# Performance work log

Measured on AMD Instinct MI355X. Metric: run time of the kernel, lower is better.

Reference implementation:

```python
import jax, jax.numpy as jnp
import numpy as np

B, T, D_MODEL = 2, 2048, 1024
H, D_HEAD, R = 16, 64, 16
CAUSAL = True


def setup_inputs() -> dict:
    key = jax.random.key(0)
    ks = jax.random.split(key, 6)
    return {
        "x": jax.random.normal(ks[0], (B, T, D_MODEL), dtype=jnp.float32),
        "W_qkv": jax.random.normal(ks[1], (D_MODEL, 3 * D_MODEL), dtype=jnp.float32) * 0.02,
        "W_q_lsr": jax.random.normal(ks[2], (H, D_HEAD, R), dtype=jnp.float32) * 0.1,
        "W_k_lsr": jax.random.normal(ks[3], (H, D_HEAD, R), dtype=jnp.float32) * 0.1,
        "core": jax.random.normal(ks[4], (H, R), dtype=jnp.float32),
        "W_o": jax.random.normal(ks[5], (D_MODEL, D_MODEL), dtype=jnp.float32) * 0.02,
    }


def reference(x, W_qkv, W_q_lsr, W_k_lsr, core, W_o):
    Bx, Tx, D = x.shape
    Hh, Dh, Rr = W_q_lsr.shape
    # Fused QKV projection, then split heads -> (B, H, T, D_head)
    qkv = x @ W_qkv  # (B, T, 3D)
    q, k, v = jnp.split(qkv, 3, axis=-1)
    q = q.reshape(Bx, Tx, Hh, Dh).transpose(0, 2, 1, 3)
    k = k.reshape(Bx, Tx, Hh, Dh).transpose(0, 2, 1, 3)
    v = v.reshape(Bx, Tx, Hh, Dh).transpose(0, 2, 1, 3)
    # Low-rank (LSR) projections of q and k; core + 1/sqrt(R) scaling on q side
    scale = 1.0 / jnp.sqrt(jnp.asarray(max(Rr, 1), dtype=jnp.float32))
    q_lr = jnp.einsum('bhtd,hdr->bhtr', q, W_q_lsr) * core[None, :, None, :] * scale
    k_lr = jnp.einsum('bhtd,hdr->bhtr', k, W_k_lsr)
    # Low-rank scores (B, H, T, T)
    scores = jnp.einsum('bhir,bhjr->bhij', q_lr, k_lr)
    if CAUSAL:
        mask = jnp.tril(jnp.ones((Tx, Tx), dtype=bool))
        scores = jnp.where(mask[None, None], scores, -jnp.inf)
    attn = jax.nn.softmax(scores, axis=-1)
    out = jnp.einsum('bhij,bhjd->bhid', attn, v)  # (B, H, T, D_head)
    out = out.transpose(0, 2, 1, 3).reshape(Bx, Tx, D)
    return out @ W_o
```

## Files before the change

### kernel.cpp

```cpp
#include <hip/hip_runtime.h>
#include <hip/hip_bf16.h>

#define BB 2
#define TT 2048
#define DD 1024
#define HH 16
#define DH 64
#define RR 16
#define BT (BB*TT)
#define BH (BB*HH)
#define D3 (3*DD)
#define NC 1536

typedef __bf16 bf16x8 __attribute__((ext_vector_type(8)));
typedef float f32x4 __attribute__((ext_vector_type(4)));
typedef short short4v __attribute__((ext_vector_type(4)));

__device__ __forceinline__ float bf2f(unsigned short u) {
  unsigned int v = ((unsigned int)u) << 16;
  return __builtin_bit_cast(float, v);
}
__device__ __forceinline__ unsigned short f2bf(float f) {
  unsigned int x = __builtin_bit_cast(unsigned int, f);
  unsigned int r = x + 0x7fffu + ((x >> 16) & 1u);
  return (unsigned short)(r >> 16);
}
__device__ __forceinline__ short4v pack_bf16x4(float a, float b, float c, float d) {
  uint2 u;
  u.x = (unsigned)f2bf(a) | ((unsigned)f2bf(b) << 16);
  u.y = (unsigned)f2bf(c) | ((unsigned)f2bf(d) << 16);
  return __builtin_bit_cast(short4v, u);
}

#define NEG_BIG (-1e30f)

__device__ __forceinline__ void async_copy16(const void* g, void* l) {
  __builtin_amdgcn_global_load_lds((const __attribute__((address_space(1))) void*)g,
                                   (__attribute__((address_space(3))) void*)l, 16, 0, 0);
}

__global__ __launch_bounds__(256) void cvt_f32_bf16(const float* __restrict__ in,
                                                    unsigned short* __restrict__ out,
                                                    int n) {
  int i = (blockIdx.x * 256 + threadIdx.x) * 8;
  if (i >= n) return;
  float4 a = *(const float4*)&in[i];
  float4 b = *(const float4*)&in[i + 4];
  unsigned short t[8] = {f2bf(a.x), f2bf(a.y), f2bf(a.z), f2bf(a.w),
                         f2bf(b.x), f2bf(b.y), f2bf(b.z), f2bf(b.w)};
  *(uint4*)&out[i] = *(const uint4*)t;
}

__global__ __launch_bounds__(256) void transpose_cvt(const float* __restrict__ in,
                                                     unsigned short* __restrict__ out,
                                                     int R, int C, int coff) {
  __shared__ float tile[32][33];
  const int tx = threadIdx.x, ty = threadIdx.y;
  const int x = blockIdx.x * 32 + tx;
  const int y0 = blockIdx.y * 32;
#pragma unroll
  for (int i = 0; i < 32; i += 8)
    tile[ty + i][tx] = in[(size_t)(y0 + ty + i) * C + coff + x];
  __syncthreads();
  const int xo = y0 + tx;
  const int yo0 = blockIdx.x * 32;
#pragma unroll
  for (int i = 0; i < 32; i += 8)
    out[(size_t)(yo0 + ty + i) * R + xo] = f2bf(tile[tx][ty + i]);
}

__global__ __launch_bounds__(256) void build_lsr(const float* __restrict__ Wqkv,
                                                 const float* __restrict__ Wql,
                                                 const float* __restrict__ Wkl,
                                                 const float* __restrict__ core,
                                                 unsigned short* __restrict__ Wcomb_t) {
  const int d0 = blockIdx.x * 64, h = blockIdx.y, tid = threadIdx.x;
  __shared__ float Aq[64][65], Ak[64][65], Lq[64][16], Lk[64][16], cs[16];
#pragma unroll
  for (int p = 0; p < 16; p++) {
    int idx = p * 256 + tid, dd = idx >> 6, e = idx & 63;
    Aq[dd][e] = Wqkv[(size_t)(d0 + dd) * D3 + h * 64 + e];
    Ak[dd][e] = Wqkv[(size_t)(d0 + dd) * D3 + DD + h * 64 + e];
  }
#pragma unroll
  for (int p = 0; p < 4; p++) {
    int idx = p * 256 + tid, e = idx >> 4, r = idx & 15;
    Lq[e][r] = Wql[h * 1024 + e * 16 + r];
    Lk[e][r] = Wkl[h * 1024 + e * 16 + r];
  }
  if (tid < 16) cs[tid] = core[h * 16 + tid];
  __syncthreads();
  const int dd = tid & 63, rg = tid >> 6;
  float aq[4] = {}, ak[4] = {};
  for (int e = 0; e < 64; e++) {
    float xq = Aq[dd][e], xk = Ak[dd][e];
#pragma unroll
    for (int j = 0; j < 4; j++) {
      aq[j] += xq * Lq[e][rg * 4 + j];
      ak[j] += xk * Lk[e][rg * 4 + j];
    }
  }
#pragma unroll
  for (int j = 0; j < 4; j++) {
    int r = rg * 4 + j;
    Wcomb_t[(size_t)(1024 + h * 16 + r) * DD + d0 + dd] = f2bf(aq[j] * cs[r] * 0.25f);
    Wcomb_t[(size_t)(1280 + h * 16 + r) * DD + d0 + dd] = f2bf(ak[j]);
  }
}

__device__ __forceinline__ void gemm64_core(const unsigned short* __restrict__ A,
                                            const unsigned short* __restrict__ Bt,
                                            int K, int bm, int bn,
                                            int tid, int g, int c, int wm, int wn,
                                            f32x4 acc[2][4]) {
  __shared__ __attribute__((aligned(16))) unsigned short As[64 * 32];
  __shared__ __attribute__((aligned(16))) unsigned short Bs[128 * 32];
  const int e0 = tid * 8;
  const int r0 = e0 >> 5, q0 = e0 & 31;
  const unsigned short* Arow = &A[(size_t)(bm * 64 + r0) * K + q0];
  const unsigned short* Brow0 = &Bt[(size_t)(bn * 128 + r0) * K + q0];
  const unsigned short* Brow1 = &Bt[(size_t)(bn * 128 + 64 + r0) * K + q0];
  for (int k0 = 0; k0 < K; k0 += 32) {
    __syncthreads();
    async_copy16(Arow + k0, &As[e0]);
    async_copy16(Brow0 + k0, &Bs[e0]);
    async_copy16(Brow1 + k0, &Bs[2048 + e0]);
    __syncthreads();
    bf16x8 af[2];
#pragma unroll
    for (int mt = 0; mt < 2; mt++)
      af[mt] = *(const bf16x8*)&As[(wm * 32 + mt * 16 + c) * 32 + g * 8];
#pragma unroll
    for (int nt = 0; nt < 4; nt++) {
      bf16x8 bf = *(const bf16x8*)&Bs[(wn * 64 + nt * 16 + c) * 32 + g * 8];
#pragma unroll
      for (int mt = 0; mt < 2; mt++)
        acc[mt][nt] = __builtin_amdgcn_mfma_f32_16x16x32_bf16(af[mt], bf, acc[mt][nt], 0, 0, 0);
    }
  }
}

__global__ __launch_bounds__(256) void gemm64_f32(const unsigned short* __restrict__ A,
                                                  const unsigned short* __restrict__ Bt,
                                                  float* __restrict__ C,
                                                  int M, int N, int K) {
  const int tid = threadIdx.x, lane = tid & 63;
  const int g = lane >> 4, c = lane & 15;
  const int wid = tid >> 6, wm = wid >> 1, wn = wid & 1;
  const int bm = blockIdx.y, bn = blockIdx.x;
  f32x4 acc[2][4] = {};
  gemm64_core(A, Bt, K, bm, bn, tid, g, c, wm, wn, acc);
#pragma unroll
  for (int mt = 0; mt < 2; mt++)
#pragma unroll
    for (int nt = 0; nt < 4; nt++)
#pragma unroll
      for (int r = 0; r < 4; r++) {
        int row = bm * 64 + wm * 32 + mt * 16 + g * 4 + r;
        int col = bn * 128 + wn * 64 + nt * 16 + c;
        C[(size_t)row * N + col] = acc[mt][nt][r];
      }
}

__global__ __launch_bounds__(256) void gemm_fused(const unsigned short* __restrict__ A,
                                                  const unsigned short* __restrict__ Bt,
                                                  unsigned short* __restrict__ qls,
                                                  unsigned short* __restrict__ klr,
                                                  unsigned short* __restrict__ vt,
                                                  int M, int N, int K) {
  const int tid = threadIdx.x, lane = tid & 63;
  const int g = lane >> 4, c = lane & 15;
  const int wid = tid >> 6, wm = wid >> 1, wn = wid & 1;
  const int bm = blockIdx.y, bn = blockIdx.x;
  f32x4 acc[2][4] = {};
  gemm64_core(A, Bt, K, bm, bn, tid, g, c, wm, wn, acc);
#pragma unroll
  for (int mt = 0; mt < 2; mt++)
#pragma unroll
    for (int nt = 0; nt < 4; nt++) {
      int colb = bn * 128 + wn * 64 + nt * 16;
      int tg0 = bm * 64 + wm * 32 + mt * 16 + g * 4;
      int b = tg0 >> 11, t0 = tg0 & 2047;
      if (colb < 1024) {
        int h = colb >> 6, d = (colb & 63) + c;
        uint2 pk = __builtin_bit_cast(uint2, pack_bf16x4(acc[mt][nt][0], acc[mt][nt][1],
                                                         acc[mt][nt][2], acc[mt][nt][3]));
        size_t idx = (size_t)(b * 16 + h) * (TT / 4) * 256 + (size_t)(t0 >> 2) * 256 + d * 4;
        *(uint2*)&vt[idx] = pk;
      } else if (colb < 1280) {
        int h = (colb - 1024) >> 4;
        size_t base = (size_t)(b * 16 + h) * TT;
#pragma unroll
        for (int r = 0; r < 4; r++)
          qls[(base + t0 + r) * 16 + c] = f2bf(acc[mt][nt][r]);
      } else {
        int h = (colb - 1280) >> 4;
        size_t base = (size_t)(b * 16 + h) * TT;
#pragma unroll
        for (int r = 0; r < 4; r++)
          klr[(base + t0 + r) * 16 + c] = f2bf(acc[mt][nt][r]);
      }
    }
}

__global__ __launch_bounds__(256, 2) void flash_lsr(const unsigned short* __restrict__ qls,
                                                    const unsigned short* __restrict__ klr,
                                                    const unsigned short* __restrict__ vt,
                                                    unsigned short* __restrict__ attn) {
  const int z = blockIdx.x;
  const int bh = blockIdx.y, b = bh >> 4, h = bh & 15;
  const int tid = threadIdx.x, lane = tid & 63, w = tid >> 6;
  const int g = lane >> 4, c = lane & 15;
  const int q0_[2] = {(31 - z) * 64, z * 64};
  const int jmax_[2] = {(31 - z) >> 1, z >> 1};

  __shared__ __attribute__((aligned(16))) unsigned short Ks[2][128 * 20];
  __shared__ __attribute__((aligned(16))) unsigned short Vs[2][32 * 264];

  const size_t qbase = (size_t)bh * TT;
  short4v qf_[2];
  int qg_[2];
  float mi_[2], li_[2];
  f32x4 oa_[2][4] = {};
#pragma unroll
  for (int t = 0; t < 2; t++) {
    qf_[t] = __builtin_bit_cast(short4v,
        *(const uint2*)&qls[(qbase + q0_[t] + w * 16 + c) * 16 + g * 4]);
    qg_[t] = q0_[t] + w * 16 + c;
    mi_[t] = NEG_BIG;
    li_[t] = 0.f;
  }
  const f32x4 zero = {0.f, 0.f, 0.f, 0.f};
  const size_t kb = (size_t)bh * TT * 16;
  const size_t vb = (size_t)bh * TT * 64;
  const int srcl = g * 16 + g * 4;

  uint4 kr = *(const uint4*)&klr[kb + tid * 8];
  uint4 vr[4];
#pragma unroll
  for (int p = 0; p < 4; p++)
    vr[p] = *(const uint4*)&vt[vb + (p * 256 + tid) * 8];

  int p = 0;
  f32x4 s_[2][8];

  auto stage = [&](int jt) {
    *(uint4*)&Ks[p][(tid >> 1) * 20 + (tid & 1) * 8] = kr;
#pragma unroll
    for (int q = 0; q < 4; q++) {
      int e = (q * 256 + tid) * 8;
      *(uint4*)&Vs[p][(e >> 8) * 264 + (e & 255)] = vr[q];
    }
    __syncthreads();
    if (jt < jmax_[0]) {
      kr = *(const uint4*)&klr[kb + (size_t)(jt + 1) * 2048 + tid * 8];
      const unsigned short* vp = &vt[vb + (size_t)(jt + 1) * 8192];
#pragma unroll
      for (int q = 0; q < 4; q++)
        vr[q] = *(const uint4*)&vp[(q * 256 + tid) * 8];
    }
  };
  auto qk = [&](int t) {
    const unsigned short* Kb = Ks[p];
#pragma unroll
    for (int nt = 0; nt < 8; nt++) {
      short4v kf = __builtin_bit_cast(short4v, *(const uint2*)&Kb[(nt * 16 + c) * 20 + g * 4]);
      s_[t][nt] = __builtin_amdgcn_mfma_f32_16x16x16bf16_1k(kf, qf_[t], zero, 0, 0, 0);
    }
  };
  auto msk = [&](int t, int jt) {
#pragma unroll
    for (int nt = 0; nt < 8; nt++)
#pragma unroll
      for (int r = 0; r < 4; r++) {
        int jg = jt * 128 + nt * 16 + g * 4 + r;
        if (jg > qg_[t]) s_[t][nt][r] = NEG_BIG;
      }
  };
  auto smax = [&](int t) {
    f32x4 vm = s_[t][0];
#pragma unroll
    for (int nt = 1; nt < 8; nt++)
#pragma unroll
      for (int r = 0; r < 4; r++) vm[r] = fmaxf(vm[r], s_[t][nt][r]);
    float rm = fmaxf(fmaxf(vm[0], vm[1]), fmaxf(vm[2], vm[3]));
    rm = fmaxf(rm, __shfl_xor(rm, 16, 64));
    rm = fmaxf(rm, __shfl_xor(rm, 32, 64));
    float mnew = fmaxf(mi_[t], rm);
    float alpha = __expf(mi_[t] - mnew);
    mi_[t] = mnew;
    f32x4 vs = zero;
#pragma unroll
    for (int nt = 0; nt < 8; nt++)
#pragma unroll
      for (int r = 0; r < 4; r++) {
        float pv = __expf(s_[t][nt][r] - mnew);
        s_[t][nt][r] = pv;
        vs[r] += pv;
      }
    float rs = (vs[0] + vs[1]) + (vs[2] + vs[3]);
    rs += __shfl_xor(rs, 16, 64);
    rs += __shfl_xor(rs, 32, 64);
    li_[t] = li_[t] * alpha + rs;
    float av[4];
#pragma unroll
    for (int r = 0; r < 4; r++) av[r] = __shfl(alpha, srcl + r, 64);
#pragma unroll
    for (int nd = 0; nd < 4; nd++)
#pragma unroll
      for (int r = 0; r < 4; r++) oa_[t][nd][r] *= av[r];
  };
  auto pv = [&](int t) {
    const unsigned short* Vb = Vs[p];
#pragma unroll
    for (int kc = 0; kc < 8; kc++) {
      short4v af = pack_bf16x4(s_[t][kc][0], s_[t][kc][1], s_[t][kc][2], s_[t][kc][3]);
#pragma unroll
      for (int nd = 0; nd < 4; nd++) {
        uint2 vv = *(const uint2*)&Vb[(kc * 4 + g) * 264 + (nd * 16 + c) * 4];
        short4v vf = __builtin_bit_cast(short4v, vv);
        oa_[t][nd] = __builtin_amdgcn_mfma_f32_16x16x16bf16_1k(af, vf, oa_[t][nd], 0, 0, 0);
      }
    }
  };

  int jt = 0;
  for (; jt <= jmax_[1]; jt++) {
    stage(jt);
    qk(0); qk(1);
    if (jt == jmax_[1]) msk(1, jt);
    smax(0); smax(1);
    pv(0); pv(1);
    p ^= 1;
  }
  for (; jt <= jmax_[0]; jt++) {
    stage(jt);
    qk(0);
    if (jt == jmax_[0]) msk(0, jt);
    smax(0);
    pv(0);
    p ^= 1;
  }

#pragma unroll
  for (int t = 0; t < 2; t++) {
    float inv = 1.f / li_[t];
    float iv[4];
#pragma unroll
    for (int r = 0; r < 4; r++) iv[r] = __shfl(inv, srcl + r, 64);
#pragma unroll
    for (int r = 0; r < 4; r++) {
      size_t rowb = ((size_t)b * TT + q0_[t] + w * 16 + g * 4 + r) * DD + h * 64;
#pragma unroll
      for (int nd = 0; nd < 4; nd++)
        attn[rowb + nd * 16 + c] = f2bf(oa_[t][nd][r] * iv[r]);
    }
  }
}

extern "C" void kernel_launch(void* const* d_in, const int* in_sizes, int n_in,
                              void* d_out, int out_size, void* d_ws, size_t ws_size,
                              hipStream_t stream) {
  const float* x      = (const float*)d_in[0];
  const float* W_qkv  = (const float*)d_in[1];
  const float* W_qlsr = (const float*)d_in[2];
  const float* W_klsr = (const float*)d_in[3];
  const float* core   = (const float*)d_in[4];
  const float* W_o    = (const float*)d_in[5];
  float* out = (float*)d_out;

  char* ws = (char*)d_ws;
  unsigned short* x_bf    = (unsigned short*)ws; ws += (size_t)BT * DD * 2;
  unsigned short* Wcomb_t = (unsigned short*)ws; ws += (size_t)NC * DD * 2;
  unsigned short* Wo_t    = (unsigned short*)ws; ws += (size_t)DD * DD * 2;
  unsigned short* qls     = (unsigned short*)ws; ws += (size_t)BH * TT * 16 * 2;
  unsigned short* klr     = (unsigned short*)ws; ws += (size_t)BH * TT * 16 * 2;
  unsigned short* vt      = (unsigned short*)ws; ws += (size_t)BH * TT * 64 * 2;
  unsigned short* attn    = (unsigned short*)ws; ws += (size_t)BT * DD * 2;

  cvt_f32_bf16<<<(BT * DD) / (256 * 8), 256, 0, stream>>>(x, x_bf, BT * DD);
  transpose_cvt<<<dim3(32, 32), dim3(32, 8), 0, stream>>>(W_o, Wo_t, DD, DD, 0);
  transpose_cvt<<<dim3(32, 32), dim3(32, 8), 0, stream>>>(W_qkv, Wcomb_t, DD, D3, 2048);
  build_lsr<<<dim3(16, 16), 256, 0, stream>>>(W_qkv, W_qlsr, W_klsr, core, Wcomb_t);
  gemm_fused<<<dim3(NC / 128, BT / 64), 256, 0, stream>>>(x_bf, Wcomb_t, qls, klr, vt, BT, NC, DD);
  flash_lsr<<<dim3(16, BH), 256, 0, stream>>>(qls, klr, vt, attn);
  gemm64_f32<<<dim3(DD / 128, BT / 64), 256, 0, stream>>>(attn, Wo_t, out, BT, DD, DD);
}
```

Measured before the change: 196.6 us.

## Split paired-query flash blocks into one tile per block, heavy first, exp2 softmax

The attention kernel previously processed two query tiles per block (a long and a short causal pair) for load balancing. It now launches one block per 64-row query tile, ordered longest-first across all batch-heads, and raises launch bounds to 3 blocks per SM. It also folds log2(e) into the q-side weight so the softmax can use the exp2 intrinsic directly. The aim is better occupancy and fewer registers per block, at the cost of reloading each K/V tile once per query tile instead of once per pair.

```diff
diff --git a/kernel.cpp b/kernel.cpp
--- a/kernel.cpp
+++ b/kernel.cpp
@@ -103,7 +103,8 @@
 #pragma unroll
   for (int j = 0; j < 4; j++) {
     int r = rg * 4 + j;
-    Wcomb_t[(size_t)(1024 + h * 16 + r) * DD + d0 + dd] = f2bf(aq[j] * cs[r] * 0.25f);
+    Wcomb_t[(size_t)(1024 + h * 16 + r) * DD + d0 + dd] =
+        f2bf(aq[j] * cs[r] * (0.25f * 1.4426950408889634f));
     Wcomb_t[(size_t)(1280 + h * 16 + r) * DD + d0 + dd] = f2bf(ak[j]);
   }
 }
@@ -203,37 +204,29 @@
     }
 }
 
-__global__ __launch_bounds__(256, 2) void flash_lsr(const unsigned short* __restrict__ qls,
+__global__ __launch_bounds__(256, 3) void flash_lsr(const unsigned short* __restrict__ qls,
                                                     const unsigned short* __restrict__ klr,
                                                     const unsigned short* __restrict__ vt,
                                                     unsigned short* __restrict__ attn) {
-  const int z = blockIdx.x;
-  const int bh = blockIdx.y, b = bh >> 4, h = bh & 15;
+  const int bh = blockIdx.x & 31, b = bh >> 4, h = bh & 15;
+  const int qt = 31 - (blockIdx.x >> 5);
   const int tid = threadIdx.x, lane = tid & 63, w = tid >> 6;
   const int g = lane >> 4, c = lane & 15;
-  const int q0_[2] = {(31 - z) * 64, z * 64};
-  const int jmax_[2] = {(31 - z) >> 1, z >> 1};
+  const int q0 = qt * 64, jmax = qt >> 1;
 
   __shared__ __attribute__((aligned(16))) unsigned short Ks[2][128 * 20];
   __shared__ __attribute__((aligned(16))) unsigned short Vs[2][32 * 264];
 
   const size_t qbase = (size_t)bh * TT;
-  short4v qf_[2];
-  int qg_[2];
-  float mi_[2], li_[2];
-  f32x4 oa_[2][4] = {};
-#pragma unroll
-  for (int t = 0; t < 2; t++) {
-    qf_[t] = __builtin_bit_cast(short4v,
-        *(const uint2*)&qls[(qbase + q0_[t] + w * 16 + c) * 16 + g * 4]);
-    qg_[t] = q0_[t] + w * 16 + c;
-    mi_[t] = NEG_BIG;
-    li_[t] = 0.f;
-  }
+  const short4v qf = __builtin_bit_cast(short4v,
+      *(const uint2*)&qls[(qbase + q0 + w * 16 + c) * 16 + g * 4]);
+  const int qg = q0 + w * 16 + c;
+  float mi = NEG_BIG, li = 0.f;
+  f32x4 oa[4] = {};
   const f32x4 zero = {0.f, 0.f, 0.f, 0.f};
   const size_t kb = (size_t)bh * TT * 16;
   const size_t vb = (size_t)bh * TT * 64;
-  const int srcl = g * 16 + g * 4;
+  const int srcl = g * 20;
 
   uint4 kr = *(const uint4*)&klr[kb + tid * 8];
   uint4 vr[4];
@@ -242,9 +235,8 @@
     vr[p] = *(const uint4*)&vt[vb + (p * 256 + tid) * 8];
 
   int p = 0;
-  f32x4 s_[2][8];
-
-  auto stage = [&](int jt) {
+  f32x4 s[8];
+  for (int jt = 0; jt <= jmax; jt++) {
     *(uint4*)&Ks[p][(tid >> 1) * 20 + (tid & 1) * 8] = kr;
 #pragma unroll
     for (int q = 0; q < 4; q++) {
@@ -252,109 +244,83 @@
       *(uint4*)&Vs[p][(e >> 8) * 264 + (e & 255)] = vr[q];
     }
     __syncthreads();
-    if (jt < jmax_[0]) {
+    if (jt < jmax) {
       kr = *(const uint4*)&klr[kb + (size_t)(jt + 1) * 2048 + tid * 8];
       const unsigned short* vp = &vt[vb + (size_t)(jt + 1) * 8192];
 #pragma unroll
       for (int q = 0; q < 4; q++)
         vr[q] = *(const uint4*)&vp[(q * 256 + tid) * 8];
     }
-  };
-  auto qk = [&](int t) {
     const unsigned short* Kb = Ks[p];
 #pragma unroll
     for (int nt = 0; nt < 8; nt++) {
       short4v kf = __builtin_bit_cast(short4v, *(const uint2*)&Kb[(nt * 16 + c) * 20 + g * 4]);
-      s_[t][nt] = __builtin_amdgcn_mfma_f32_16x16x16bf16_1k(kf, qf_[t], zero, 0, 0, 0);
-    }
-  };
-  auto msk = [&](int t, int jt) {
-#pragma unroll
-    for (int nt = 0; nt < 8; nt++)
-#pragma unroll
-      for (int r = 0; r < 4; r++) {
-        int jg = jt * 128 + nt * 16 + g * 4 + r;
-        if (jg > qg_[t]) s_[t][nt][r] = NEG_BIG;
-      }
-  };
-  auto smax = [&](int t) {
-    f32x4 vm = s_[t][0];
+      s[nt] = __builtin_amdgcn_mfma_f32_16x16x16bf16_1k(kf, qf, zero, 0, 0, 0);
+    }
+    if (jt == jmax) {
+#pragma unroll
+      for (int nt = 0; nt < 8; nt++)
+#pragma unroll
+        for (int r = 0; r < 4; r++) {
+          int jg = jt * 128 + nt * 16 + g * 4 + r;
+          if (jg > qg) s[nt][r] = NEG_BIG;
+        }
+    }
+    f32x4 vm = s[0];
 #pragma unroll
     for (int nt = 1; nt < 8; nt++)
 #pragma unroll
-      for (int r = 0; r < 4; r++) vm[r] = fmaxf(vm[r], s_[t][nt][r]);
+      for (int r = 0; r < 4; r++) vm[r] = fmaxf(vm[r], s[nt][r]);
     float rm = fmaxf(fmaxf(vm[0], vm[1]), fmaxf(vm[2], vm[3]));
     rm = fmaxf(rm, __shfl_xor(rm, 16, 64));
     rm = fmaxf(rm, __shfl_xor(rm, 32, 64));
-    float mnew = fmaxf(mi_[t], rm);
-    float alpha = __expf(mi_[t] - mnew);
-    mi_[t] = mnew;
+    float mnew = fmaxf(mi, rm);
+    float alpha = __builtin_amdgcn_exp2f(mi - mnew);
+    mi = mnew;
     f32x4 vs = zero;
 #pragma unroll
     for (int nt = 0; nt < 8; nt++)
 #pragma unroll
       for (int r = 0; r < 4; r++) {
-        float pv = __expf(s_[t][nt][r] - mnew);
-        s_[t][nt][r] = pv;
+        float pv = __builtin_amdgcn_exp2f(s[nt][r] - mnew);
+        s[nt][r] = pv;
         vs[r] += pv;
       }
     float rs = (vs[0] + vs[1]) + (vs[2] + vs[3]);
     rs += __shfl_xor(rs, 16, 64);
     rs += __shfl_xor(rs, 32, 64);
-    li_[t] = li_[t] * alpha + rs;
+    li = li * alpha + rs;
     float av[4];
 #pragma unroll
     for (int r = 0; r < 4; r++) av[r] = __shfl(alpha, srcl + r, 64);
 #pragma unroll
     for (int nd = 0; nd < 4; nd++)
 #pragma unroll
-      for (int r = 0; r < 4; r++) oa_[t][nd][r] *= av[r];
-  };
-  auto pv = [&](int t) {
+      for (int r = 0; r < 4; r++) oa[nd][r] *= av[r];
     const unsigned short* Vb = Vs[p];
 #pragma unroll
     for (int kc = 0; kc < 8; kc++) {
-      short4v af = pack_bf16x4(s_[t][kc][0], s_[t][kc][1], s_[t][kc][2], s_[t][kc][3]);
+      short4v af = pack_bf16x4(s[kc][0], s[kc][1], s[kc][2], s[kc][3]);
 #pragma unroll
       for (int nd = 0; nd < 4; nd++) {
         uint2 vv = *(const uint2*)&Vb[(kc * 4 + g) * 264 + (nd * 16 + c) * 4];
         short4v vf = __builtin_bit_cast(short4v, vv);
-        oa_[t][nd] = __builtin_amdgcn_mfma_f32_16x16x16bf16_1k(af, vf, oa_[t][nd], 0, 0, 0);
+        oa[nd] = __builtin_amdgcn_mfma_f32_16x16x16bf16_1k(af, vf, oa[nd], 0, 0, 0);
       }
     }
-  };
-
-  int jt = 0;
-  for (; jt <= jmax_[1]; jt++) {
-    stage(jt);
-    qk(0); qk(1);
-    if (jt == jmax_[1]) msk(1, jt);
-    smax(0); smax(1);
-    pv(0); pv(1);
     p ^= 1;
   }
-  for (; jt <= jmax_[0]; jt++) {
-    stage(jt);
-    qk(0);
-    if (jt == jmax_[0]) msk(0, jt);
-    smax(0);
-    pv(0);
-    p ^= 1;
-  }
-
-#pragma unroll
-  for (int t = 0; t < 2; t++) {
-    float inv = 1.f / li_[t];
-    float iv[4];
-#pragma unroll
-    for (int r = 0; r < 4; r++) iv[r] = __shfl(inv, srcl + r, 64);
-#pragma unroll
-    for (int r = 0; r < 4; r++) {
-      size_t rowb = ((size_t)b * TT + q0_[t] + w * 16 + g * 4 + r) * DD + h * 64;
-#pragma unroll
-      for (int nd = 0; nd < 4; nd++)
-        attn[rowb + nd * 16 + c] = f2bf(oa_[t][nd][r] * iv[r]);
-    }
+
+  float inv = 1.f / li;
+  float iv[4];
+#pragma unroll
+  for (int r = 0; r < 4; r++) iv[r] = __shfl(inv, srcl + r, 64);
+#pragma unroll
+  for (int r = 0; r < 4; r++) {
+    size_t rowb = ((size_t)b * TT + q0 + w * 16 + g * 4 + r) * DD + h * 64;
+#pragma unroll
+    for (int nd = 0; nd < 4; nd++)
+      attn[rowb + nd * 16 + c] = f2bf(oa[nd][r] * iv[r]);
   }
 }
 
@@ -383,6 +349,6 @@
   transpose_cvt<<<dim3(32, 32), dim3(32, 8), 0, stream>>>(W_qkv, Wcomb_t, DD, D3, 2048);
   build_lsr<<<dim3(16, 16), 256, 0, stream>>>(W_qkv, W_qlsr, W_klsr, core, Wcomb_t);
   gemm_fused<<<dim3(NC / 128, BT / 64), 256, 0, stream>>>(x_bf, Wcomb_t, qls, klr, vt, BT, NC, DD);
-  flash_lsr<<<dim3(16, BH), 256, 0, stream>>>(qls, klr, vt, attn);
+  flash_lsr<<<dim3(32 * BH), 256, 0, stream>>>(qls, klr, vt, attn);
   gemm64_f32<<<dim3(DD / 128, BT / 64), 256, 0, stream>>>(attn, Wo_t, out, BT, DD, DD);
 }
```

Result: no change. 193.0 us (-1.8%).
